# Kernel optimization log

Hardware: AMD Instinct MI355X
Metric: run time of the kernel (lower is better)

Reference implementation:

```python
import jax, jax.numpy as jnp
import numpy as np
from jax.ops import segment_sum, segment_max

N = 50000        # nodes
E = 800000       # edges (before self loops)
IN_DIM = 128
HID = 16         # per-head out channels
HEADS = 4
NL = 3           # num GAT layers
OUT = 1
NG = 128         # number of graphs in the batch
NEG = 0.2        # LeakyReLU negative slope (PyG GATConv default)
EPS = 1e-5       # BatchNorm eps


def setup_inputs() -> dict:
    key = jax.random.key(0)
    ks = iter(jax.random.split(key, 64))
    inp = {}
    inp['x'] = jax.random.normal(next(ks), (N, IN_DIM), jnp.float32)
    inp['edge_index'] = jax.random.randint(next(ks), (2, E), 0, N, dtype=jnp.int32)
    inp['batch'] = jnp.sort(jax.random.randint(next(ks), (N,), 0, NG, dtype=jnp.int32))
    d = IN_DIM
    for l in range(NL):
        s = 1.0 / np.sqrt(d)
        inp[f'W{l}'] = jax.random.uniform(next(ks), (HEADS * HID, d), jnp.float32, -s, s)
        inp[f'att_src{l}'] = jax.random.normal(next(ks), (HEADS, HID), jnp.float32) * 0.1
        inp[f'att_dst{l}'] = jax.random.normal(next(ks), (HEADS, HID), jnp.float32) * 0.1
        inp[f'bias{l}'] = jnp.zeros((HEADS * HID,), jnp.float32)
        inp[f'gamma{l}'] = jnp.ones((HEADS * HID,), jnp.float32)
        inp[f'beta{l}'] = jnp.zeros((HEADS * HID,), jnp.float32)
        inp[f'mean{l}'] = jax.random.normal(next(ks), (HEADS * HID,), jnp.float32) * 0.1
        inp[f'var{l}'] = jax.random.uniform(next(ks), (HEADS * HID,), jnp.float32, 0.5, 1.5)
        d = HEADS * HID
    s = 1.0 / np.sqrt(d)
    inp['fcW'] = jax.random.uniform(next(ks), (OUT, d), jnp.float32, -s, s)
    inp['fcb'] = jnp.zeros((OUT,), jnp.float32)
    return inp


def gat_layer(x, src, dst, W, att_src, att_dst, bias):
    """PyG GATConv (concat=True). src/dst already include self loops."""
    n = x.shape[0]
    h = (x @ W.T).reshape(n, HEADS, HID)            # [N,H,C]
    a_s = jnp.sum(h * att_src, axis=-1)             # [N,H]
    a_d = jnp.sum(h * att_dst, axis=-1)             # [N,H]
    logits = a_s[src] + a_d[dst]                    # [Etot,H]
    logits = jnp.where(logits > 0, logits, NEG * logits)  # leaky_relu
    # scatter-softmax over destination-node neighborhoods
    m = segment_max(logits, dst, num_segments=n)
    e = jnp.exp(logits - m[dst])
    z = segment_sum(e, dst, num_segments=n)
    alpha = e / z[dst]                              # [Etot,H]
    out = segment_sum(h[src] * alpha[:, :, None], dst, num_segments=n)  # [N,H,C]
    return out.reshape(n, HEADS * HID) + bias, alpha


def reference(x, edge_index, batch,
              W0, att_src0, att_dst0, bias0, gamma0, beta0, mean0, var0,
              W1, att_src1, att_dst1, bias1, gamma1, beta1, mean1, var1,
              W2, att_src2, att_dst2, bias2, gamma2, beta2, mean2, var2,
              fcW, fcb):
    n = x.shape[0]
    loops = jnp.arange(n, dtype=edge_index.dtype)   # add_self_loops=True
    src = jnp.concatenate([edge_index[0], loops])
    dst = jnp.concatenate([edge_index[1], loops])
    params = [
        (W0, att_src0, att_dst0, bias0, gamma0, beta0, mean0, var0),
        (W1, att_src1, att_dst1, bias1, gamma1, beta1, mean1, var1),
        (W2, att_src2, att_dst2, bias2, gamma2, beta2, mean2, var2),
    ]
    h = x
    alpha0 = None
    for l, (W, a_s, a_d, b, g, be, mu, var) in enumerate(params):
        h, alpha = gat_layer(h, src, dst, W, a_s, a_d, b)
        if l == 0:
            alpha0 = alpha
        h = jax.nn.relu(h)
        h = g * (h - mu) / jnp.sqrt(var + EPS) + be  # BatchNorm1d (eval); dropout = identity
    # global_mean_pool over graph ids
    sums = segment_sum(h, batch, num_segments=NG)
    cnt = segment_sum(jnp.ones((n, 1), h.dtype), batch, num_segments=NG)
    pooled = sums / jnp.maximum(cnt, 1.0)
    out = jax.nn.sigmoid(pooled @ fcW.T + fcb)      # [NG, OUT]
    return out, alpha0
```

## Files before the change

### kernel.cpp

```cpp
#include <hip/hip_runtime.h>
#include <hip/hip_fp16.h>
#include <math.h>

#define NN     50000
#define EE     800000
#define ETOT   (EE + NN)
#define INDIM  128
#define HEADS  4
#define NG     128
#define NEGS   0.2f
#define BNEPS  1e-5f

typedef _Float16 half8 __attribute__((ext_vector_type(8)));
typedef _Float16 half4v __attribute__((ext_vector_type(4)));
typedef float floatx4 __attribute__((ext_vector_type(4)));


__global__ void degree_kernel(const int* __restrict__ ei, int* __restrict__ deg,
                              int* __restrict__ rank) {
    int e = blockIdx.x * blockDim.x + threadIdx.x;
    if (e >= ETOT) return;
    int d = (e < EE) ? ei[EE + e] : (e - EE);
    rank[e] = atomicAdd(&deg[d], 1);
}

__global__ void scan_block_kernel(const int* __restrict__ deg, int* __restrict__ rowstart,
                                  int* __restrict__ bsums) {
    __shared__ int tmp[1024];
    int tid = threadIdx.x;
    int i = blockIdx.x * 1024 + tid;
    int v = (i < NN) ? deg[i] : 0;
    tmp[tid] = v;
    __syncthreads();
    for (int off = 1; off < 1024; off <<= 1) {
        int t = (tid >= off) ? tmp[tid - off] : 0;
        __syncthreads();
        tmp[tid] += t;
        __syncthreads();
    }
    if (i < NN) rowstart[i] = tmp[tid] - v;
    if (tid == 1023) bsums[blockIdx.x] = tmp[tid];
}

__global__ void add_offsets_kernel(int* __restrict__ rowstart, const int* __restrict__ bsums) {
    int i = blockIdx.x * blockDim.x + threadIdx.x;
    if (i == 0) rowstart[NN] = ETOT;
    if (i >= NN) return;
    int nbk = i >> 10;
    int off = 0;
    for (int j = 0; j < nbk; ++j) off += bsums[j];
    rowstart[i] += off;
}

__global__ void scatter_kernel(const int* __restrict__ ei, const int* __restrict__ rowstart,
                               const int* __restrict__ rank, int* __restrict__ csr) {
    int e = blockIdx.x * blockDim.x + threadIdx.x;
    if (e >= ETOT) return;
    int s, d;
    if (e < EE) { s = ei[e]; d = ei[EE + e]; }
    else        { s = e - EE; d = e - EE; }
    int pos = rowstart[d] + rank[e];
    csr[pos] = s;
}

#define NX8 (NN * INDIM / 8)
#define PREP_TOT (NX8 + 2048 + NN + NG * 64 + NG)
__global__ __launch_bounds__(256) void prep_kernel(const float* __restrict__ x,
                                                   const float* __restrict__ W0,
                                                   const float* __restrict__ W1,
                                                   const float* __restrict__ W2,
                                                   _Float16* __restrict__ Xh,
                                                   _Float16* __restrict__ Wh,
                                                   int* __restrict__ deg,
                                                   float* __restrict__ psums,
                                                   int* __restrict__ pcnt) {
    int i = blockIdx.x * blockDim.x + threadIdx.x;
    if (i < NX8) {
        float4 v0 = *(const float4*)(x + (size_t)i * 8);
        float4 v1 = *(const float4*)(x + (size_t)i * 8 + 4);
        half8 o;
        o[0] = (_Float16)v0.x; o[1] = (_Float16)v0.y;
        o[2] = (_Float16)v0.z; o[3] = (_Float16)v0.w;
        o[4] = (_Float16)v1.x; o[5] = (_Float16)v1.y;
        o[6] = (_Float16)v1.z; o[7] = (_Float16)v1.w;
        *(half8*)(Xh + (size_t)i * 8) = o;
    } else if (i < NX8 + 2048) {
        int wi = (i - NX8) * 8;
#pragma unroll
        for (int j = 0; j < 8; ++j) {
            int idx = wi + j;
            float v = (idx < 8192) ? W0[idx]
                    : ((idx < 12288) ? W1[idx - 8192] : W2[idx - 12288]);
            Wh[idx] = (_Float16)v;
        }
    } else if (i < NX8 + 2048 + NN) {
        deg[i - NX8 - 2048] = 0;
    } else if (i < NX8 + 2048 + NN + NG * 64) {
        psums[i - NX8 - 2048 - NN] = 0.f;
    } else if (i < PREP_TOT) {
        pcnt[i - NX8 - 2048 - NN - NG * 64] = 0;
    }
}

template <int DD>
__global__ __launch_bounds__(256) void gemm_att_kernel(
    const _Float16* __restrict__ X, const _Float16* __restrict__ Wh,
    const float* __restrict__ attS, const float* __restrict__ attD,
    _Float16* __restrict__ H, float* __restrict__ AS, float* __restrict__ AD) {
    constexpr int KB = DD / 32;
    int tid = threadIdx.x;
    int wv = tid >> 6;
    int lane = tid & 63;
    int quad = lane >> 4;
    int n = lane & 15;
    int wbase = blockIdx.x * 64 + wv * 16;

    int arow = wbase + n;
    if (arow >= NN) arow = NN - 1;
    half8 a[KB];
#pragma unroll
    for (int kb = 0; kb < KB; ++kb)
        a[kb] = *(const half8*)(X + (size_t)arow * DD + kb * 32 + quad * 8);

    floatx4 c[4];
#pragma unroll
    for (int t = 0; t < 4; ++t) {
        floatx4 acc = {0.f, 0.f, 0.f, 0.f};
#pragma unroll
        for (int kb = 0; kb < KB; ++kb) {
            half8 b = *(const half8*)(Wh + (size_t)(t * 16 + n) * DD + kb * 32 + quad * 8);
            acc = __builtin_amdgcn_mfma_f32_16x16x32_f16(a[kb], b, acc, 0, 0, 0);
        }
        c[t] = acc;
    }

    float as_l[4], ad_l[4];
#pragma unroll
    for (int t = 0; t < 4; ++t) {
        as_l[t] = attS[t * 16 + n];
        ad_l[t] = attD[t * 16 + n];
    }
#pragma unroll
    for (int r = 0; r < 4; ++r) {
        int node = wbase + quad * 4 + r;
        bool ok = node < NN;
#pragma unroll
        for (int t = 0; t < 4; ++t) {
            float h = c[t][r];
            if (ok) H[(size_t)node * 64 + t * 16 + n] = (_Float16)h;
            float vs = h * as_l[t];
            float vd = h * ad_l[t];
#pragma unroll
            for (int off = 8; off; off >>= 1) {
                vs += __shfl_down(vs, off, 16);
                vd += __shfl_down(vd, off, 16);
            }
            if (ok && n == 0) {
                AS[node * 4 + t] = vs;
                AD[node * 4 + t] = vd;
            }
        }
    }
}

template <bool WRITE_Z>
__global__ __launch_bounds__(256) void edge_aggr_kernel(
    const _Float16* __restrict__ H, const float* __restrict__ AS,
    const float* __restrict__ AD,
    const int* __restrict__ rowstart,
    const int* __restrict__ csr,
    const float* __restrict__ bias, const float* __restrict__ gamma,
    const float* __restrict__ beta, const float* __restrict__ mean,
    const float* __restrict__ var, _Float16* __restrict__ Hout,
    float* __restrict__ Z) {
    int v = (blockIdx.x * blockDim.x + threadIdx.x) >> 6;
    if (v >= NN) return;
    int lane = threadIdx.x & 63;
    int q = lane >> 4;
    int l16 = lane & 15;
    int head = l16 >> 2;
    int ch4 = l16 * 4;
    float adv = AD[v * 4 + head];
    int start = rowstart[v];
    int cnt = rowstart[v + 1] - start;
    const int* srow = csr + start;
    float z = 0.f;
    float acc0 = 0.f, acc1 = 0.f, acc2 = 0.f, acc3 = 0.f;
    int k = 0;
    for (; k + 16 <= cnt; k += 16) {
        int b = k + q * 4;
        int s0 = srow[b + 0];
        int s1 = srow[b + 1];
        int s2 = srow[b + 2];
        int s3 = srow[b + 3];
        float a0 = AS[(size_t)s0 * 4 + head];
        float a1 = AS[(size_t)s1 * 4 + head];
        float a2 = AS[(size_t)s2 * 4 + head];
        float a3 = AS[(size_t)s3 * 4 + head];
        half4v h0 = *(const half4v*)(H + (size_t)s0 * 64 + ch4);
        half4v h1 = *(const half4v*)(H + (size_t)s1 * 64 + ch4);
        half4v h2 = *(const half4v*)(H + (size_t)s2 * 64 + ch4);
        half4v h3 = *(const half4v*)(H + (size_t)s3 * 64 + ch4);
        float l0 = a0 + adv; l0 = l0 > 0.f ? l0 : NEGS * l0; float p0 = __expf(l0);
        float l1 = a1 + adv; l1 = l1 > 0.f ? l1 : NEGS * l1; float p1 = __expf(l1);
        float l2 = a2 + adv; l2 = l2 > 0.f ? l2 : NEGS * l2; float p2 = __expf(l2);
        float l3 = a3 + adv; l3 = l3 > 0.f ? l3 : NEGS * l3; float p3 = __expf(l3);
        z += (p0 + p1) + (p2 + p3);
        acc0 = fmaf(p0, (float)h0[0], acc0); acc1 = fmaf(p0, (float)h0[1], acc1);
        acc2 = fmaf(p0, (float)h0[2], acc2); acc3 = fmaf(p0, (float)h0[3], acc3);
        acc0 = fmaf(p1, (float)h1[0], acc0); acc1 = fmaf(p1, (float)h1[1], acc1);
        acc2 = fmaf(p1, (float)h1[2], acc2); acc3 = fmaf(p1, (float)h1[3], acc3);
        acc0 = fmaf(p2, (float)h2[0], acc0); acc1 = fmaf(p2, (float)h2[1], acc1);
        acc2 = fmaf(p2, (float)h2[2], acc2); acc3 = fmaf(p2, (float)h2[3], acc3);
        acc0 = fmaf(p3, (float)h3[0], acc0); acc1 = fmaf(p3, (float)h3[1], acc1);
        acc2 = fmaf(p3, (float)h3[2], acc2); acc3 = fmaf(p3, (float)h3[3], acc3);
    }
    for (; k < cnt; k += 4) {
        int idx = k + q;
        if (idx < cnt) {
            int s = srow[idx];
            float a = AS[(size_t)s * 4 + head];
            half4v hv = *(const half4v*)(H + (size_t)s * 64 + ch4);
            float l = a + adv; l = l > 0.f ? l : NEGS * l;
            float p = __expf(l);
            z += p;
            acc0 = fmaf(p, (float)hv[0], acc0);
            acc1 = fmaf(p, (float)hv[1], acc1);
            acc2 = fmaf(p, (float)hv[2], acc2);
            acc3 = fmaf(p, (float)hv[3], acc3);
        }
    }
    z    += __shfl_xor(z, 16);    z    += __shfl_xor(z, 32);
    acc0 += __shfl_xor(acc0, 16); acc0 += __shfl_xor(acc0, 32);
    acc1 += __shfl_xor(acc1, 16); acc1 += __shfl_xor(acc1, 32);
    acc2 += __shfl_xor(acc2, 16); acc2 += __shfl_xor(acc2, 32);
    acc3 += __shfl_xor(acc3, 16); acc3 += __shfl_xor(acc3, 32);
    if (q == 0) {
        if (WRITE_Z && (l16 & 3) == 0) Z[v * 4 + head] = z;
        float4 bi = *(const float4*)(bias + ch4);
        float4 ga = *(const float4*)(gamma + ch4);
        float4 be = *(const float4*)(beta + ch4);
        float4 mu = *(const float4*)(mean + ch4);
        float4 va = *(const float4*)(var + ch4);
        float r0 = fmaxf(acc0 / z + bi.x, 0.f);
        float r1 = fmaxf(acc1 / z + bi.y, 0.f);
        float r2 = fmaxf(acc2 / z + bi.z, 0.f);
        float r3 = fmaxf(acc3 / z + bi.w, 0.f);
        r0 = ga.x * (r0 - mu.x) * rsqrtf(va.x + BNEPS) + be.x;
        r1 = ga.y * (r1 - mu.y) * rsqrtf(va.y + BNEPS) + be.y;
        r2 = ga.z * (r2 - mu.z) * rsqrtf(va.z + BNEPS) + be.z;
        r3 = ga.w * (r3 - mu.w) * rsqrtf(va.w + BNEPS) + be.w;
        half4v o;
        o[0] = (_Float16)r0;
        o[1] = (_Float16)r1;
        o[2] = (_Float16)r2;
        o[3] = (_Float16)r3;
        *(half4v*)(Hout + (size_t)v * 64 + ch4) = o;
    }
}

__global__ __launch_bounds__(256) void alpha_kernel(
    const int* __restrict__ ei,
    const float* __restrict__ AS, const float* __restrict__ AD,
    const float* __restrict__ Z, float* __restrict__ alpha_out) {
    int e = blockIdx.x * blockDim.x + threadIdx.x;
    if (e >= ETOT) return;
    int s, d;
    if (e < EE) { s = ei[e]; d = ei[EE + e]; }
    else        { s = e - EE; d = e - EE; }
    float4 as = *(const float4*)(AS + (size_t)s * 4);
    float4 ad = *(const float4*)(AD + (size_t)d * 4);
    float4 z4 = *(const float4*)(Z + (size_t)d * 4);
    float l;
    float4 a;
    l = as.x + ad.x; l = l > 0.f ? l : NEGS * l; a.x = __expf(l) / z4.x;
    l = as.y + ad.y; l = l > 0.f ? l : NEGS * l; a.y = __expf(l) / z4.y;
    l = as.z + ad.z; l = l > 0.f ? l : NEGS * l; a.z = __expf(l) / z4.z;
    l = as.w + ad.w; l = l > 0.f ? l : NEGS * l; a.w = __expf(l) / z4.w;
    *(float4*)(alpha_out + (size_t)e * 4) = a;
}

__global__ __launch_bounds__(256) void pool_kernel(const __half* __restrict__ H,
                                                   const int* __restrict__ batch,
                                                   float* __restrict__ sums,
                                                   int* __restrict__ cnt) {
    int wid = (blockIdx.x * blockDim.x + threadIdx.x) >> 6;
    int lane = threadIdx.x & 63;
    int base = wid * 64;
    if (base >= NN) return;
    int end = min(base + 64, NN);
    int cur = batch[base];
    float acc = 0.f;
    int c0 = 0;
    for (int i = base; i < end; ++i) {
        int g = batch[i];
        if (g != cur) {
            atomicAdd(&sums[cur * 64 + lane], acc);
            if (lane == 0) atomicAdd(&cnt[cur], c0);
            cur = g; acc = 0.f; c0 = 0;
        }
        acc += __half2float(H[(size_t)i * 64 + lane]);
        c0++;
    }
    atomicAdd(&sums[cur * 64 + lane], acc);
    if (lane == 0) atomicAdd(&cnt[cur], c0);
}

__global__ void fc_kernel(const float* __restrict__ sums, const int* __restrict__ cnt,
                          const float* __restrict__ fcW, const float* __restrict__ fcb,
                          float* __restrict__ out) {
    int g = (blockIdx.x * blockDim.x + threadIdx.x) >> 6;
    int lane = threadIdx.x & 63;
    if (g >= NG) return;
    float c = fmaxf((float)cnt[g], 1.f);
    float val = (sums[g * 64 + lane] / c) * fcW[lane];
#pragma unroll
    for (int off = 32; off; off >>= 1) val += __shfl_down(val, off, 64);
    if (lane == 0) out[g] = 1.f / (1.f + expf(-(val + fcb[0])));
}

extern "C" void kernel_launch(void* const* d_in, const int* in_sizes, int n_in,
                              void* d_out, int out_size, void* d_ws, size_t ws_size,
                              hipStream_t stream) {
    const float* x   = (const float*)d_in[0];
    const int* ei    = (const int*)d_in[1];
    const int* batch = (const int*)d_in[2];
    const float* W[3], *attS[3], *attD[3], *bias[3], *gamma[3], *beta[3], *mean[3], *var[3];
    for (int l = 0; l < 3; ++l) {
        W[l]     = (const float*)d_in[3 + 8 * l + 0];
        attS[l]  = (const float*)d_in[3 + 8 * l + 1];
        attD[l]  = (const float*)d_in[3 + 8 * l + 2];
        bias[l]  = (const float*)d_in[3 + 8 * l + 3];
        gamma[l] = (const float*)d_in[3 + 8 * l + 4];
        beta[l]  = (const float*)d_in[3 + 8 * l + 5];
        mean[l]  = (const float*)d_in[3 + 8 * l + 6];
        var[l]   = (const float*)d_in[3 + 8 * l + 7];
    }
    const float* fcW = (const float*)d_in[27];
    const float* fcb = (const float*)d_in[28];
    float* out = (float*)d_out;
    float* alpha_out = (float*)d_out + NG;

    char* p = (char*)d_ws;
    auto carve = [&](size_t bytes) {
        char* q = p;
        p += (bytes + 255) & ~(size_t)255;
        return q;
    };
    _Float16* Xh    = (_Float16*)carve(sizeof(_Float16) * NN * INDIM);
    _Float16* Wh    = (_Float16*)carve(sizeof(_Float16) * 16384);
    _Float16* Hh    = (_Float16*)carve(sizeof(_Float16) * NN * 64);
    _Float16* Hn    = (_Float16*)carve(sizeof(_Float16) * NN * 64);
    float* AS       = (float*)carve(sizeof(float) * NN * 4);
    float* AD       = (float*)carve(sizeof(float) * NN * 4);
    float* Z        = (float*)carve(sizeof(float) * NN * 4);
    int*   rowstart = (int*)carve(sizeof(int) * (NN + 1));
    int*   deg      = (int*)carve(sizeof(int) * NN);
    int*   rank     = (int*)carve(sizeof(int) * ETOT);
    int*   bsums    = (int*)carve(sizeof(int) * 64);
    int*   csr      = (int*)carve(sizeof(int) * ETOT);
    float* psums    = (float*)carve(sizeof(float) * NG * 64);
    int*   pcnt     = (int*)carve(sizeof(int) * NG);

    prep_kernel<<<(PREP_TOT + 255) / 256, 256, 0, stream>>>(
        x, W[0], W[1], W[2], Xh, Wh, deg, psums, pcnt);

    int nbScan = (NN + 1023) / 1024;
    degree_kernel<<<(ETOT + 255) / 256, 256, 0, stream>>>(ei, deg, rank);
    scan_block_kernel<<<nbScan, 1024, 0, stream>>>(deg, rowstart, bsums);
    add_offsets_kernel<<<(NN + 255) / 256, 256, 0, stream>>>(rowstart, bsums);
    scatter_kernel<<<(ETOT + 255) / 256, 256, 0, stream>>>(ei, rowstart, rank, csr);

    int edgeBlocks = (NN * 64 + 255) / 256;
    int posBlocks = (ETOT + 255) / 256;
    int gemmBlocks = (NN + 63) / 64;

    gemm_att_kernel<128><<<gemmBlocks, 256, 0, stream>>>(Xh, Wh, attS[0], attD[0],
                                                         Hh, AS, AD);
    edge_aggr_kernel<true><<<edgeBlocks, 256, 0, stream>>>(
        Hh, AS, AD, rowstart, csr,
        bias[0], gamma[0], beta[0], mean[0], var[0], Hn, Z);
    alpha_kernel<<<posBlocks, 256, 0, stream>>>(ei, AS, AD, Z, alpha_out);

    gemm_att_kernel<64><<<gemmBlocks, 256, 0, stream>>>(Hn, Wh + 8192, attS[1], attD[1],
                                                        Hh, AS, AD);
    edge_aggr_kernel<false><<<edgeBlocks, 256, 0, stream>>>(
        Hh, AS, AD, rowstart, csr,
        bias[1], gamma[1], beta[1], mean[1], var[1], Hn, nullptr);

    gemm_att_kernel<64><<<gemmBlocks, 256, 0, stream>>>(Hn, Wh + 12288, attS[2], attD[2],
                                                        Hh, AS, AD);
    edge_aggr_kernel<false><<<edgeBlocks, 256, 0, stream>>>(
        Hh, AS, AD, rowstart, csr,
        bias[2], gamma[2], beta[2], mean[2], var[2], Hn, nullptr);

    int poolWaves = (NN + 63) / 64;
    pool_kernel<<<(poolWaves * 64 + 255) / 256, 256, 0, stream>>>(
        (const __half*)Hn, batch, psums, pcnt);
    fc_kernel<<<(NG * 64 + 255) / 256, 256, 0, stream>>>(psums, pcnt, fcW, fcb, out);
}
```

Before: 364.4 us.

## Overlap CSR construction and alpha output with GEMM via a second stream

Splits the prep kernel into a zeroing kernel and a conversion kernel. CSR building (degree, scan, scatter) now runs on a second non-blocking stream while the fp16 conversion and first GEMM run on the main stream, joined by events. The layer-0 alpha kernel also runs on the second stream, concurrent with layers 1-2, which get their own AS/AD buffers so they do not overwrite the arrays alpha still reads. Streams and events are created on every call and never destroyed, which adds host overhead and leaks resources.

```diff
diff --git a/kernel.cpp b/kernel.cpp
--- a/kernel.cpp
+++ b/kernel.cpp
@@ -63,17 +63,22 @@
     csr[pos] = s;
 }
 
-#define NX8 (NN * INDIM / 8)
-#define PREP_TOT (NX8 + 2048 + NN + NG * 64 + NG)
-__global__ __launch_bounds__(256) void prep_kernel(const float* __restrict__ x,
-                                                   const float* __restrict__ W0,
-                                                   const float* __restrict__ W1,
-                                                   const float* __restrict__ W2,
-                                                   _Float16* __restrict__ Xh,
-                                                   _Float16* __restrict__ Wh,
-                                                   int* __restrict__ deg,
+__global__ __launch_bounds__(256) void zero_kernel(int* __restrict__ deg,
                                                    float* __restrict__ psums,
                                                    int* __restrict__ pcnt) {
+    int i = blockIdx.x * blockDim.x + threadIdx.x;
+    if (i < NN) deg[i] = 0;
+    else if (i < NN + NG * 64) psums[i - NN] = 0.f;
+    else if (i < NN + NG * 64 + NG) pcnt[i - NN - NG * 64] = 0;
+}
+
+#define NX8 (NN * INDIM / 8)
+__global__ __launch_bounds__(256) void cvt_kernel(const float* __restrict__ x,
+                                                  const float* __restrict__ W0,
+                                                  const float* __restrict__ W1,
+                                                  const float* __restrict__ W2,
+                                                  _Float16* __restrict__ Xh,
+                                                  _Float16* __restrict__ Wh) {
     int i = blockIdx.x * blockDim.x + threadIdx.x;
     if (i < NX8) {
         float4 v0 = *(const float4*)(x + (size_t)i * 8);
@@ -93,12 +98,6 @@
                     : ((idx < 12288) ? W1[idx - 8192] : W2[idx - 12288]);
             Wh[idx] = (_Float16)v;
         }
-    } else if (i < NX8 + 2048 + NN) {
-        deg[i - NX8 - 2048] = 0;
-    } else if (i < NX8 + 2048 + NN + NG * 64) {
-        psums[i - NX8 - 2048 - NN] = 0.f;
-    } else if (i < PREP_TOT) {
-        pcnt[i - NX8 - 2048 - NN - NG * 64] = 0;
     }
 }
 
@@ -351,8 +350,10 @@
     _Float16* Wh    = (_Float16*)carve(sizeof(_Float16) * 16384);
     _Float16* Hh    = (_Float16*)carve(sizeof(_Float16) * NN * 64);
     _Float16* Hn    = (_Float16*)carve(sizeof(_Float16) * NN * 64);
-    float* AS       = (float*)carve(sizeof(float) * NN * 4);
-    float* AD       = (float*)carve(sizeof(float) * NN * 4);
+    float* AS0      = (float*)carve(sizeof(float) * NN * 4);
+    float* AD0      = (float*)carve(sizeof(float) * NN * 4);
+    float* AS1      = (float*)carve(sizeof(float) * NN * 4);
+    float* AD1      = (float*)carve(sizeof(float) * NN * 4);
     float* Z        = (float*)carve(sizeof(float) * NN * 4);
     int*   rowstart = (int*)carve(sizeof(int) * (NN + 1));
     int*   deg      = (int*)carve(sizeof(int) * NN);
@@ -362,38 +363,54 @@
     float* psums    = (float*)carve(sizeof(float) * NG * 64);
     int*   pcnt     = (int*)carve(sizeof(int) * NG);
 
-    prep_kernel<<<(PREP_TOT + 255) / 256, 256, 0, stream>>>(
-        x, W[0], W[1], W[2], Xh, Wh, deg, psums, pcnt);
-
-    int nbScan = (NN + 1023) / 1024;
-    degree_kernel<<<(ETOT + 255) / 256, 256, 0, stream>>>(ei, deg, rank);
-    scan_block_kernel<<<nbScan, 1024, 0, stream>>>(deg, rowstart, bsums);
-    add_offsets_kernel<<<(NN + 255) / 256, 256, 0, stream>>>(rowstart, bsums);
-    scatter_kernel<<<(ETOT + 255) / 256, 256, 0, stream>>>(ei, rowstart, rank, csr);
+    hipStream_t s2;
+    hipStreamCreateWithFlags(&s2, hipStreamNonBlocking);
+    hipEvent_t evFork, evCsr, evAggr0, evAlpha;
+    hipEventCreateWithFlags(&evFork, hipEventDisableTiming);
+    hipEventCreateWithFlags(&evCsr, hipEventDisableTiming);
+    hipEventCreateWithFlags(&evAggr0, hipEventDisableTiming);
+    hipEventCreateWithFlags(&evAlpha, hipEventDisableTiming);
 
     int edgeBlocks = (NN * 64 + 255) / 256;
     int posBlocks = (ETOT + 255) / 256;
     int gemmBlocks = (NN + 63) / 64;
-
+    int nbScan = (NN + 1023) / 1024;
+
+    hipEventRecord(evFork, stream);
+    hipStreamWaitEvent(s2, evFork, 0);
+    zero_kernel<<<(NN + NG * 64 + NG + 255) / 256, 256, 0, s2>>>(deg, psums, pcnt);
+    degree_kernel<<<(ETOT + 255) / 256, 256, 0, s2>>>(ei, deg, rank);
+    scan_block_kernel<<<nbScan, 1024, 0, s2>>>(deg, rowstart, bsums);
+    add_offsets_kernel<<<(NN + 255) / 256, 256, 0, s2>>>(rowstart, bsums);
+    scatter_kernel<<<(ETOT + 255) / 256, 256, 0, s2>>>(ei, rowstart, rank, csr);
+    hipEventRecord(evCsr, s2);
+
+    cvt_kernel<<<(NX8 + 2048 + 255) / 256, 256, 0, stream>>>(x, W[0], W[1], W[2], Xh, Wh);
     gemm_att_kernel<128><<<gemmBlocks, 256, 0, stream>>>(Xh, Wh, attS[0], attD[0],
-                                                         Hh, AS, AD);
+                                                         Hh, AS0, AD0);
+    hipStreamWaitEvent(stream, evCsr, 0);
+
     edge_aggr_kernel<true><<<edgeBlocks, 256, 0, stream>>>(
-        Hh, AS, AD, rowstart, csr,
+        Hh, AS0, AD0, rowstart, csr,
         bias[0], gamma[0], beta[0], mean[0], var[0], Hn, Z);
-    alpha_kernel<<<posBlocks, 256, 0, stream>>>(ei, AS, AD, Z, alpha_out);
+    hipEventRecord(evAggr0, stream);
+    hipStreamWaitEvent(s2, evAggr0, 0);
+    alpha_kernel<<<posBlocks, 256, 0, s2>>>(ei, AS0, AD0, Z, alpha_out);
+    hipEventRecord(evAlpha, s2);
 
     gemm_att_kernel<64><<<gemmBlocks, 256, 0, stream>>>(Hn, Wh + 8192, attS[1], attD[1],
-                                                        Hh, AS, AD);
+                                                        Hh, AS1, AD1);
     edge_aggr_kernel<false><<<edgeBlocks, 256, 0, stream>>>(
-        Hh, AS, AD, rowstart, csr,
+        Hh, AS1, AD1, rowstart, csr,
         bias[1], gamma[1], beta[1], mean[1], var[1], Hn, nullptr);
 
     gemm_att_kernel<64><<<gemmBlocks, 256, 0, stream>>>(Hn, Wh + 12288, attS[2], attD[2],
-                                                        Hh, AS, AD);
+                                                        Hh, AS1, AD1);
     edge_aggr_kernel<false><<<edgeBlocks, 256, 0, stream>>>(
-        Hh, AS, AD, rowstart, csr,
+        Hh, AS1, AD1, rowstart, csr,
         bias[2], gamma[2], beta[2], mean[2], var[2], Hn, nullptr);
 
+    hipStreamWaitEvent(stream, evAlpha, 0);
     int poolWaves = (NN + 63) / 64;
     pool_kernel<<<(poolWaves * 64 + 255) / 256, 256, 0, stream>>>(
         (const __half*)Hn, batch, psums, pcnt);
```

Measured after the change: 416.5 us. 14.3% more time.
